# Kernel tuning notes

Measured on AMD Instinct MI355X. Metric: run time of the kernel, lower is better.

Reference implementation:

```python
import jax, jax.numpy as jnp
import numpy as np

B, S, D, H = 256, 128, 1024, 8
DH = D // H  # per-head dim = input_length / head


def setup_inputs() -> dict:
    key = jax.random.key(0)
    ks = jax.random.split(key, 12)
    code = jax.random.normal(ks[0], (B, S, D), dtype=jnp.float32)
    # 0/1 adjacency (PDG relation mask)
    input_relation = jax.random.bernoulli(ks[1], 0.2, (B, S, S)).astype(jnp.float32)
    w = 0.02
    Wq = jax.random.normal(ks[2], (H, D, DH), dtype=jnp.float32) * w
    bq = jnp.zeros((H, DH), dtype=jnp.float32)
    Wk = jax.random.normal(ks[3], (H, D, DH), dtype=jnp.float32) * w
    bk = jnp.zeros((H, DH), dtype=jnp.float32)
    Wv = jax.random.normal(ks[4], (H, D, DH), dtype=jnp.float32) * w
    bv = jnp.zeros((H, DH), dtype=jnp.float32)
    Wo = jax.random.normal(ks[5], (2 * D, D), dtype=jnp.float32) * w
    bo = jnp.zeros((D,), dtype=jnp.float32)
    return {"code": code, "input_relation": input_relation,
            "Wq": Wq, "bq": bq, "Wk": Wk, "bk": bk,
            "Wv": Wv, "bv": bv, "Wo": Wo, "bo": bo}


def reference(code, input_relation, Wq, bq, Wk, bk, Wv, bv, Wo, bo):
    Hn = Wq.shape[0]
    half = Hn // 2
    Sn = code.shape[1]
    E = jnp.eye(Sn, dtype=code.dtype)
    # Faithful to the TF loop: head i < H/2 sees relation + i*I (the loop
    # reassigns input_relation = this_relation + I each iteration);
    # heads i >= H/2 see the ORIGINAL transposed relation.
    i_idx = jnp.arange(half, dtype=code.dtype)  # [half]
    rel_fwd = input_relation[None] + i_idx[:, None, None, None] * E  # [half,B,S,S]
    rel_t = jnp.swapaxes(input_relation, 1, 2)
    rel_bwd = jnp.broadcast_to(rel_t[None], (Hn - half,) + rel_t.shape)
    rels = jnp.concatenate([rel_fwd, rel_bwd], axis=0)  # [H,B,S,S]

    relu = jax.nn.relu
    Q = relu(jnp.einsum('bsd,hdf->hbsf', code, Wq) + bq[:, None, None, :])
    K = relu(jnp.einsum('bsd,hdf->hbsf', code, Wk) + bk[:, None, None, :])
    V = relu(jnp.einsum('bsd,hdf->hbsf', code, Wv) + bv[:, None, None, :])

    attn = jnp.einsum('hbsf,hbtf->hbst', Q, K)  # [H,B,S,S]
    pdg = rels * attn + 1e-11
    # tf.reduce_sum axis=1 (rows) -> our axis=2; axis=2 (cols) -> our axis=3
    indeg = jnp.sqrt(jnp.sum(pdg, axis=2, keepdims=True))   # [H,B,1,S]
    outdeg = jnp.sqrt(jnp.sum(pdg, axis=3, keepdims=True))  # [H,B,S,1]
    pdg = pdg / indeg / outdeg
    softed = rels * pdg
    res = jnp.einsum('hbst,hbtf->hbsf', softed, V)  # [H,B,S,DH]

    # concat heads along features (head 0 first), then concat original code
    all_ch = jnp.transpose(res, (1, 2, 0, 3)).reshape(code.shape[0], Sn, -1)
    add_ori = jnp.concatenate([all_ch, code], axis=-1)  # [B,S,2D]
    out = relu(add_ori @ Wo + bo)
    return out
```

## Files before the change

### kernel.cpp

```cpp
#include <hip/hip_runtime.h>
#include <cstdint>
#include <cstddef>

#define B_  256
#define S_  128
#define D_  1024
#define H_  8
#define DH_ 128
#define M_  (B_ * S_)

typedef _Float16 half8 __attribute__((ext_vector_type(8)));
typedef float    f32x4 __attribute__((ext_vector_type(4)));

#define GLOAD_LDS16(gp, lp)                                                    \
    __builtin_amdgcn_global_load_lds(                                          \
        (const __attribute__((address_space(1))) void*)(gp),                   \
        (__attribute__((address_space(3))) void*)(lp), 16, 0, 0)

__global__ __launch_bounds__(256)
void cvt_code(const float* __restrict__ src, _Float16* __restrict__ dst, int n8)
{
    int i = blockIdx.x * 256 + threadIdx.x;
    if (i >= n8) return;
    const float4* s = (const float4*)src;
    float4 a = s[2 * i], b = s[2 * i + 1];
    half8 o;
    o[0] = (_Float16)a.x; o[1] = (_Float16)a.y; o[2] = (_Float16)a.z; o[3] = (_Float16)a.w;
    o[4] = (_Float16)b.x; o[5] = (_Float16)b.y; o[6] = (_Float16)b.z; o[7] = (_Float16)b.w;
    *(half8*)(dst + (size_t)i * 8) = o;
}

__global__ __launch_bounds__(256)
void cvt_wqkv(const float* __restrict__ Wq, const float* __restrict__ Wk,
              const float* __restrict__ Wv,
              const float* __restrict__ bq, const float* __restrict__ bk,
              const float* __restrict__ bv,
              _Float16* __restrict__ Wt, float* __restrict__ bias_all)
{
    int idx = blockIdx.x * 256 + threadIdx.x;
    if (idx >= 3072 * 128) return;
    int n = idx >> 7, kc = idx & 127, k = kc * 8;
    int qkv = n >> 10, hf = n & 1023, h = hf >> 7, f = hf & 127;
    const float* W = (qkv == 0 ? Wq : (qkv == 1 ? Wk : Wv))
                     + (size_t)h * D_ * DH_ + (size_t)k * DH_ + f;
    half8 o;
    #pragma unroll
    for (int j = 0; j < 8; ++j) o[j] = (_Float16)W[(size_t)j * DH_];
    *(half8*)(Wt + (size_t)n * 1024 + k) = o;
    if (kc == 0)
        bias_all[n] = (qkv == 0 ? bq : (qkv == 1 ? bk : bv))[h * DH_ + f];
}

__global__ __launch_bounds__(256)
void cvt_wo(const float* __restrict__ Wo, _Float16* __restrict__ Wot)
{
    int idx = blockIdx.x * 256 + threadIdx.x;
    if (idx >= 1024 * 256) return;
    int n = idx >> 8, kc = idx & 255, k = kc * 8;
    const float* W = Wo + (size_t)k * 1024 + n;
    half8 o;
    #pragma unroll
    for (int j = 0; j < 8; ++j) o[j] = (_Float16)W[(size_t)j * 1024];
    *(half8*)(Wot + (size_t)n * 2048 + k) = o;
}

template <bool OUTF32>
__global__ __launch_bounds__(256, 2)
void gemm_f16(const _Float16* __restrict__ A1, const _Float16* __restrict__ A2,
              int K1, const _Float16* __restrict__ Bt,
              const float* __restrict__ bias, void* __restrict__ outp,
              int Ntot, int Ktot)
{
    __shared__ _Float16 Ab[2][128 * 32];
    __shared__ _Float16 Bb[2][128 * 32];

    const int tid = threadIdx.x;
    const int w = tid >> 6, l = tid & 63;
    const int wr = w >> 1, wc = w & 1;
    const int m0 = blockIdx.x * 128, n0 = blockIdx.y * 128;
    const int NT = Ktot / 32;

    auto stage = [&](int buf, int t) {
        const int k0 = t * 32;
        const _Float16* Asrc; int kc;
        if (k0 < K1) { Asrc = A1; kc = k0; } else { Asrc = A2; kc = k0 - K1; }
        const int r = w * 32 + (l >> 2);
        const int c = (l & 3) * 8;
        #pragma unroll
        for (int i = 0; i < 2; ++i) {
            const _Float16* g = Asrc + (size_t)(m0 + r + i * 16) * 1024 + kc + c;
            GLOAD_LDS16(g, &Ab[buf][(w * 32 + i * 16) * 32]);
        }
        #pragma unroll
        for (int i = 0; i < 2; ++i) {
            const _Float16* g = Bt + (size_t)(n0 + r + i * 16) * Ktot + k0 + c;
            GLOAD_LDS16(g, &Bb[buf][(w * 32 + i * 16) * 32]);
        }
    };

    f32x4 acc[4][4] = {};

    stage(0, 0);
    __syncthreads();

    int buf = 0;
    for (int t = 0; t < NT; ++t) {
        if (t + 1 < NT) stage(buf ^ 1, t + 1);

        const int g = l >> 4, r = l & 15;
        half8 af[4], bf[4];
        #pragma unroll
        for (int i = 0; i < 4; ++i)
            af[i] = *(const half8*)&Ab[buf][(wr * 64 + i * 16 + r) * 32 + g * 8];
        #pragma unroll
        for (int j = 0; j < 4; ++j)
            bf[j] = *(const half8*)&Bb[buf][(wc * 64 + j * 16 + r) * 32 + g * 8];

        #pragma unroll
        for (int i = 0; i < 4; ++i)
            #pragma unroll
            for (int j = 0; j < 4; ++j)
                acc[i][j] = __builtin_amdgcn_mfma_f32_16x16x32_f16(af[i], bf[j], acc[i][j], 0, 0, 0);

        __syncthreads();
        buf ^= 1;
    }

    const int lg = l >> 4, lr = l & 15;
    #pragma unroll
    for (int i = 0; i < 4; ++i) {
        #pragma unroll
        for (int j = 0; j < 4; ++j) {
            const int n = n0 + wc * 64 + j * 16 + lr;
            const float bs = bias[n];
            #pragma unroll
            for (int rg = 0; rg < 4; ++rg) {
                const int m = m0 + wr * 64 + i * 16 + lg * 4 + rg;
                float v = acc[i][j][rg] + bs;
                v = v > 0.0f ? v : 0.0f;
                if constexpr (OUTF32)
                    ((float*)outp)[(size_t)m * Ntot + n] = v;
                else
                    ((_Float16*)outp)[(size_t)m * Ntot + n] = (_Float16)v;
            }
        }
    }
}

#define PPAD 136
#define VPAD 40

__global__ __launch_bounds__(256, 2)
void attn_pdg_mfma(const _Float16* __restrict__ QKV, const float* __restrict__ Rel,
                   _Float16* __restrict__ resh)
{
    __shared__ __align__(16) char smem[72704];
    _Float16* P     = (_Float16*)smem;
    _Float16* Qs    = (_Float16*)(smem + 34816);
    _Float16* Ks    = Qs + 2 * 4096;
    _Float16* Vt    = (_Float16*)(smem + 34816);
    unsigned* rbits = (unsigned*)(smem + 67584);
    float* rowpart  = (float*)(smem + 69632);
    float* colpart  = (float*)(smem + 70656);
    float* inv_in   = (float*)(smem + 71680);
    float* inv_out  = (float*)(smem + 72192);

    const int tid = threadIdx.x;
    const int w = tid >> 6, l = tid & 63;
    const int wr = w >> 1, wc = w & 1;
    const int lr = l & 15, lg = l >> 4;
    const int b = blockIdx.x, h = blockIdx.y;

    for (int s = w; s < S_; s += 4) {
        const float* row = &Rel[((size_t)b * S_ + s) * S_];
        unsigned long long b0 = __ballot(row[l] > 0.5f);
        unsigned long long b1 = __ballot(row[64 + l] > 0.5f);
        if (l == 0) {
            rbits[s * 4 + 0] = (unsigned)b0; rbits[s * 4 + 1] = (unsigned)(b0 >> 32);
            rbits[s * 4 + 2] = (unsigned)b1; rbits[s * 4 + 3] = (unsigned)(b1 >> 32);
        }
    }

    const size_t gbase = (size_t)(b * S_) * 3072 + h * DH_;

    auto stageQK = [&](int bufi, int t) {
        const int k0 = t * 32;
        const int rr = l >> 2, cc = (l & 3) * 8;
        #pragma unroll
        for (int i = 0; i < 2; ++i) {
            const int row = w * 32 + i * 16;
            const _Float16* gq = QKV + gbase + (size_t)(row + rr) * 3072 + k0 + cc;
            GLOAD_LDS16(gq, Qs + bufi * 4096 + row * 32);
            const _Float16* gk = QKV + gbase + 1024 + (size_t)(row + rr) * 3072 + k0 + cc;
            GLOAD_LDS16(gk, Ks + bufi * 4096 + row * 32);
        }
    };

    f32x4 acc[4][4] = {};
    stageQK(0, 0);
    __syncthreads();
    int buf = 0;
    for (int t = 0; t < 4; ++t) {
        if (t < 3) stageQK(buf ^ 1, t + 1);
        half8 af[4], bf[4];
        #pragma unroll
        for (int i = 0; i < 4; ++i)
            af[i] = *(const half8*)&Qs[buf * 4096 + (wr * 64 + i * 16 + lr) * 32 + lg * 8];
        #pragma unroll
        for (int j = 0; j < 4; ++j)
            bf[j] = *(const half8*)&Ks[buf * 4096 + (wc * 64 + j * 16 + lr) * 32 + lg * 8];
        #pragma unroll
        for (int i = 0; i < 4; ++i)
            #pragma unroll
            for (int j = 0; j < 4; ++j)
                acc[i][j] = __builtin_amdgcn_mfma_f32_16x16x32_f16(af[i], bf[j], acc[i][j], 0, 0, 0);
        __syncthreads();
        buf ^= 1;
    }

    auto relf = [&](int s, int t) -> float {
        float r;
        if (h < H_ / 2) {
            r = (float)((rbits[s * 4 + (t >> 5)] >> (t & 31)) & 1u);
            if (s == t) r += (float)h;
        } else {
            r = (float)((rbits[t * 4 + (s >> 5)] >> (s & 31)) & 1u);
        }
        return r;
    };

    f32x4 p[4][4];
    #pragma unroll
    for (int i = 0; i < 4; ++i)
        #pragma unroll
        for (int j = 0; j < 4; ++j)
            #pragma unroll
            for (int rg = 0; rg < 4; ++rg) {
                const int s = wr * 64 + i * 16 + lg * 4 + rg;
                const int t = wc * 64 + j * 16 + lr;
                p[i][j][rg] = relf(s, t) * acc[i][j][rg] + 1e-11f;
            }

    #pragma unroll
    for (int i = 0; i < 4; ++i)
        #pragma unroll
        for (int rg = 0; rg < 4; ++rg) {
            float part = p[i][0][rg] + p[i][1][rg] + p[i][2][rg] + p[i][3][rg];
            part += __shfl_xor(part, 1);
            part += __shfl_xor(part, 2);
            part += __shfl_xor(part, 4);
            part += __shfl_xor(part, 8);
            if (lr == 0) rowpart[wc * 128 + wr * 64 + i * 16 + lg * 4 + rg] = part;
        }
    #pragma unroll
    for (int j = 0; j < 4; ++j) {
        float part = 0.0f;
        #pragma unroll
        for (int i = 0; i < 4; ++i)
            part += p[i][j][0] + p[i][j][1] + p[i][j][2] + p[i][j][3];
        part += __shfl_xor(part, 16);
        part += __shfl_xor(part, 32);
        if (lg == 0) colpart[wr * 128 + wc * 64 + j * 16 + lr] = part;
    }
    __syncthreads();

    if (tid < 128) {
        inv_in[tid] = rsqrtf(colpart[tid] + colpart[128 + tid]);
    } else {
        const int s = tid - 128;
        inv_out[s] = rsqrtf(rowpart[s] + rowpart[128 + s]);
    }
    __syncthreads();

    float itj[4];
    #pragma unroll
    for (int j = 0; j < 4; ++j) itj[j] = inv_in[wc * 64 + j * 16 + lr];
    #pragma unroll
    for (int i = 0; i < 4; ++i)
        #pragma unroll
        for (int rg = 0; rg < 4; ++rg) {
            const int s = wr * 64 + i * 16 + lg * 4 + rg;
            const float os = inv_out[s];
            #pragma unroll
            for (int j = 0; j < 4; ++j) {
                const int t = wc * 64 + j * 16 + lr;
                const float val = relf(s, t) * p[i][j][rg] * itj[j] * os;
                P[s * PPAD + t] = (_Float16)val;
            }
        }

    const _Float16* Vb = QKV + gbase + 2048;
    uint4 vreg[2];
    auto loadV = [&](int t) {
        #pragma unroll
        for (int ii = 0; ii < 2; ++ii) {
            const int unit = tid + ii * 256;
            const int tt = unit & 31, fg = unit >> 5;
            vreg[ii] = *(const uint4*)&Vb[(size_t)(t * 32 + tt) * 3072 + fg * 8];
        }
    };

    loadV(0);
    f32x4 acc2[4][4] = {};
    for (int t = 0; t < 4; ++t) {
        #pragma unroll
        for (int ii = 0; ii < 2; ++ii) {
            union { uint4 u; _Float16 hh[8]; } uu;
            uu.u = vreg[ii];
            const int unit = tid + ii * 256;
            const int tt = unit & 31, fg = unit >> 5;
            #pragma unroll
            for (int e = 0; e < 8; ++e)
                Vt[(fg * 8 + e) * VPAD + tt] = uu.hh[e];
        }
        __syncthreads();
        if (t < 3) loadV(t + 1);

        half8 af[4], bf[4];
        #pragma unroll
        for (int i = 0; i < 4; ++i)
            af[i] = *(const half8*)&P[(wr * 64 + i * 16 + lr) * PPAD + t * 32 + lg * 8];
        #pragma unroll
        for (int j = 0; j < 4; ++j)
            bf[j] = *(const half8*)&Vt[(wc * 64 + j * 16 + lr) * VPAD + lg * 8];
        #pragma unroll
        for (int i = 0; i < 4; ++i)
            #pragma unroll
            for (int j = 0; j < 4; ++j)
                acc2[i][j] = __builtin_amdgcn_mfma_f32_16x16x32_f16(af[i], bf[j], acc2[i][j], 0, 0, 0);
        __syncthreads();
    }

    #pragma unroll
    for (int i = 0; i < 4; ++i)
        #pragma unroll
        for (int rg = 0; rg < 4; ++rg) {
            const int s = wr * 64 + i * 16 + lg * 4 + rg;
            #pragma unroll
            for (int j = 0; j < 4; ++j) {
                const int f = wc * 64 + j * 16 + lr;
                resh[((size_t)(b * S_ + s)) * 1024 + h * DH_ + f] = (_Float16)acc2[i][j][rg];
            }
        }
}

extern "C" void kernel_launch(void* const* d_in, const int* in_sizes, int n_in,
                              void* d_out, int out_size, void* d_ws, size_t ws_size,
                              hipStream_t stream)
{
    const float* code = (const float*)d_in[0];
    const float* Rel  = (const float*)d_in[1];
    const float* Wq   = (const float*)d_in[2];
    const float* bq   = (const float*)d_in[3];
    const float* Wk   = (const float*)d_in[4];
    const float* bk   = (const float*)d_in[5];
    const float* Wv   = (const float*)d_in[6];
    const float* bv   = (const float*)d_in[7];
    const float* Wo   = (const float*)d_in[8];
    const float* bo   = (const float*)d_in[9];
    float* out = (float*)d_out;
    (void)in_sizes; (void)n_in; (void)out_size; (void)ws_size;

    char* wsp = (char*)d_ws;
    _Float16* codeh = (_Float16*)wsp;  wsp += (size_t)M_ * 1024 * 2;
    _Float16* QKV   = (_Float16*)wsp;  wsp += (size_t)M_ * 3072 * 2;
    _Float16* resh  = (_Float16*)wsp;  wsp += (size_t)M_ * 1024 * 2;
    _Float16* Wt    = (_Float16*)wsp;  wsp += (size_t)3072 * 1024 * 2;
    _Float16* Wot   = (_Float16*)wsp;  wsp += (size_t)1024 * 2048 * 2;
    float* bias_all = (float*)wsp;     wsp += 3072 * 4;

    cvt_code<<<(M_ * 1024 / 8 + 255) / 256, 256, 0, stream>>>(code, codeh, M_ * 1024 / 8);
    cvt_wqkv<<<(3072 * 128 + 255) / 256, 256, 0, stream>>>(Wq, Wk, Wv, bq, bk, bv, Wt, bias_all);
    cvt_wo<<<(1024 * 256 + 255) / 256, 256, 0, stream>>>(Wo, Wot);

    gemm_f16<false><<<dim3(M_ / 128, 24), 256, 0, stream>>>(
        codeh, codeh, 1024, Wt, bias_all, (void*)QKV, 3072, 1024);

    attn_pdg_mfma<<<dim3(B_, H_), 256, 0, stream>>>(QKV, Rel, resh);

    gemm_f16<true><<<dim3(M_ / 128, 8), 256, 0, stream>>>(
        resh, codeh, 1024, Wot, bo, (void*)out, 1024, 2048);
}
```

Baseline: 661.9 us.

## Rewrite fp16 GEMM as 256x256 8-wave ping-pong pipeline with swizzled LDS

Replaces the 128x128 four-wave GEMM with a 256x256 tile, 512-thread kernel using BK=64 and a 128KB double-buffered LDS. The K-step is split into four quarter-phases that interleave global-to-LDS staging with MFMA blocks, using explicit vmcnt waits, barriers and s_setprio. LDS is XOR-swizzled to avoid bank conflicts, and blocks are remapped to group tiles for better L2 reuse. This aims to raise MFMA utilization and arithmetic intensity for both projection GEMMs, at the cost of one block per CU and fragile hand-tuned wait counts.

After: 568.1 us. 14.2% less time.

```diff
diff --git a/kernel.cpp b/kernel.cpp
--- a/kernel.cpp
+++ b/kernel.cpp
@@ -65,78 +65,172 @@
 }
 
 template <bool OUTF32>
-__global__ __launch_bounds__(256, 2)
-void gemm_f16(const _Float16* __restrict__ A1, const _Float16* __restrict__ A2,
-              int K1, const _Float16* __restrict__ Bt,
-              const float* __restrict__ bias, void* __restrict__ outp,
-              int Ntot, int Ktot)
-{
-    __shared__ _Float16 Ab[2][128 * 32];
-    __shared__ _Float16 Bb[2][128 * 32];
+__global__ __launch_bounds__(512, 1)
+void gemm_f16_8p(const _Float16* __restrict__ A1p, const _Float16* __restrict__ A2p,
+                 int K1, const _Float16* __restrict__ Bt,
+                 const float* __restrict__ bias, void* __restrict__ outp,
+                 int Ntot, int Ktot, int ntn)
+{
+    __shared__ __align__(16) char lds[131072];
 
     const int tid = threadIdx.x;
     const int w = tid >> 6, l = tid & 63;
-    const int wr = w >> 1, wc = w & 1;
-    const int m0 = blockIdx.x * 128, n0 = blockIdx.y * 128;
-    const int NT = Ktot / 32;
-
-    auto stage = [&](int buf, int t) {
-        const int k0 = t * 32;
-        const _Float16* Asrc; int kc;
-        if (k0 < K1) { Asrc = A1; kc = k0; } else { Asrc = A2; kc = k0 - K1; }
-        const int r = w * 32 + (l >> 2);
-        const int c = (l & 3) * 8;
-        #pragma unroll
-        for (int i = 0; i < 2; ++i) {
-            const _Float16* g = Asrc + (size_t)(m0 + r + i * 16) * 1024 + kc + c;
-            GLOAD_LDS16(g, &Ab[buf][(w * 32 + i * 16) * 32]);
-        }
-        #pragma unroll
-        for (int i = 0; i < 2; ++i) {
-            const _Float16* g = Bt + (size_t)(n0 + r + i * 16) * Ktot + k0 + c;
-            GLOAD_LDS16(g, &Bb[buf][(w * 32 + i * 16) * 32]);
-        }
-    };
-
-    f32x4 acc[4][4] = {};
-
-    stage(0, 0);
-    __syncthreads();
-
-    int buf = 0;
+    const int wm = w >> 2, wn = w & 3;
+    const int lr = l & 15, lg = l >> 4;
+
+    const int cpx = gridDim.x >> 3;
+    const int bid = blockIdx.x;
+    const int swz = (bid & 7) * cpx + (bid >> 3);
+    const int m0 = (swz / ntn) * 256, n0 = (swz % ntn) * 256;
+
+    const int NT = Ktot >> 6;
+
+    const int srow  = l >> 3;
+    const int sgcol = ((l & 7) ^ srow) * 8;
+
+    auto stageHalf = [&](int bufi, int t, int half) {
+        const int k0 = t << 6;
+        const bool isA = (half == 0) || (half == 3);
+        const int hh = (half >= 2) ? 1 : 0;
+        char* dst0 = lds + bufi * 65536 + (isA ? 0 : 32768) + hh * 16384;
+        if (isA) {
+            const _Float16* Asrc; int kc;
+            if (k0 < K1) { Asrc = A1p; kc = k0; } else { Asrc = A2p; kc = k0 - K1; }
+            #pragma unroll
+            for (int i = 0; i < 2; ++i) {
+                const int c = i * 8 + w;
+                const int row = hh * 128 + c * 8 + srow;
+                const _Float16* g = Asrc + (size_t)(m0 + row) * 1024 + kc + sgcol;
+                GLOAD_LDS16(g, dst0 + c * 1024);
+            }
+        } else {
+            #pragma unroll
+            for (int i = 0; i < 2; ++i) {
+                const int c = i * 8 + w;
+                const int row = hh * 128 + c * 8 + srow;
+                const _Float16* g = Bt + (size_t)(n0 + row) * Ktot + k0 + sgcol;
+                GLOAD_LDS16(g, dst0 + c * 1024);
+            }
+        }
+    };
+
+    auto ldA = [&](int bufi, int fi, int ks) -> half8 {
+        const int row = fi * 32 + wm * 16 + lr;
+        const int pos = (ks * 4 + lg) ^ (row & 7);
+        return *(const half8*)(lds + bufi * 65536 + row * 128 + pos * 16);
+    };
+    auto ldB = [&](int bufi, int fj, int ks) -> half8 {
+        const int row = fj * 64 + wn * 16 + lr;
+        const int pos = (ks * 4 + lg) ^ (row & 7);
+        return *(const half8*)(lds + bufi * 65536 + 32768 + row * 128 + pos * 16);
+    };
+
+    f32x4 acc[8][4] = {};
+    half8 aq[4][2], b0[2][2], b1[2][2];
+
+    stageHalf(0, 0, 0); stageHalf(0, 0, 1); stageHalf(0, 0, 2); stageHalf(0, 0, 3);
+
     for (int t = 0; t < NT; ++t) {
-        if (t + 1 < NT) stage(buf ^ 1, t + 1);
-
-        const int g = l >> 4, r = l & 15;
-        half8 af[4], bf[4];
-        #pragma unroll
-        for (int i = 0; i < 4; ++i)
-            af[i] = *(const half8*)&Ab[buf][(wr * 64 + i * 16 + r) * 32 + g * 8];
-        #pragma unroll
-        for (int j = 0; j < 4; ++j)
-            bf[j] = *(const half8*)&Bb[buf][(wc * 64 + j * 16 + r) * 32 + g * 8];
-
-        #pragma unroll
-        for (int i = 0; i < 4; ++i)
-            #pragma unroll
-            for (int j = 0; j < 4; ++j)
-                acc[i][j] = __builtin_amdgcn_mfma_f32_16x16x32_f16(af[i], bf[j], acc[i][j], 0, 0, 0);
-
-        __syncthreads();
-        buf ^= 1;
-    }
-
-    const int lg = l >> 4, lr = l & 15;
-    #pragma unroll
-    for (int i = 0; i < 4; ++i) {
-        #pragma unroll
-        for (int j = 0; j < 4; ++j) {
-            const int n = n0 + wc * 64 + j * 16 + lr;
+        const int buf = t & 1;
+        const bool nl = (t + 1 < NT);
+
+        asm volatile("s_waitcnt vmcnt(4)" ::: "memory");
+        __builtin_amdgcn_s_barrier();
+        #pragma unroll
+        for (int fi = 0; fi < 4; ++fi)
+            #pragma unroll
+            for (int ks = 0; ks < 2; ++ks)
+                aq[fi][ks] = ldA(buf, fi, ks);
+        #pragma unroll
+        for (int fj = 0; fj < 2; ++fj)
+            #pragma unroll
+            for (int ks = 0; ks < 2; ++ks)
+                b0[fj][ks] = ldB(buf, fj, ks);
+        if (nl) stageHalf(buf ^ 1, t + 1, 0);
+        asm volatile("s_waitcnt lgkmcnt(0)" ::: "memory");
+        __builtin_amdgcn_sched_barrier(0);
+        __builtin_amdgcn_s_setprio(1);
+        #pragma unroll
+        for (int ks = 0; ks < 2; ++ks)
+            #pragma unroll
+            for (int fi = 0; fi < 4; ++fi)
+                #pragma unroll
+                for (int fj = 0; fj < 2; ++fj)
+                    acc[fi][fj] = __builtin_amdgcn_mfma_f32_16x16x32_f16(
+                        aq[fi][ks], b0[fj][ks], acc[fi][fj], 0, 0, 0);
+        __builtin_amdgcn_s_setprio(0);
+        __builtin_amdgcn_s_barrier();
+
+        if (nl) asm volatile("s_waitcnt vmcnt(4)" ::: "memory");
+        else    asm volatile("s_waitcnt vmcnt(2)" ::: "memory");
+        __builtin_amdgcn_s_barrier();
+        #pragma unroll
+        for (int fj = 0; fj < 2; ++fj)
+            #pragma unroll
+            for (int ks = 0; ks < 2; ++ks)
+                b1[fj][ks] = ldB(buf, fj + 2, ks);
+        if (nl) stageHalf(buf ^ 1, t + 1, 1);
+        asm volatile("s_waitcnt lgkmcnt(0)" ::: "memory");
+        __builtin_amdgcn_sched_barrier(0);
+        __builtin_amdgcn_s_setprio(1);
+        #pragma unroll
+        for (int ks = 0; ks < 2; ++ks)
+            #pragma unroll
+            for (int fi = 0; fi < 4; ++fi)
+                #pragma unroll
+                for (int fj = 0; fj < 2; ++fj)
+                    acc[fi][fj + 2] = __builtin_amdgcn_mfma_f32_16x16x32_f16(
+                        aq[fi][ks], b1[fj][ks], acc[fi][fj + 2], 0, 0, 0);
+        __builtin_amdgcn_s_setprio(0);
+        __builtin_amdgcn_s_barrier();
+
+        if (nl) asm volatile("s_waitcnt vmcnt(4)" ::: "memory");
+        else    asm volatile("s_waitcnt vmcnt(0)" ::: "memory");
+        __builtin_amdgcn_s_barrier();
+        #pragma unroll
+        for (int fi = 0; fi < 4; ++fi)
+            #pragma unroll
+            for (int ks = 0; ks < 2; ++ks)
+                aq[fi][ks] = ldA(buf, fi + 4, ks);
+        if (nl) stageHalf(buf ^ 1, t + 1, 2);
+        asm volatile("s_waitcnt lgkmcnt(0)" ::: "memory");
+        __builtin_amdgcn_sched_barrier(0);
+        __builtin_amdgcn_s_setprio(1);
+        #pragma unroll
+        for (int ks = 0; ks < 2; ++ks)
+            #pragma unroll
+            for (int fi = 0; fi < 4; ++fi)
+                #pragma unroll
+                for (int fj = 0; fj < 2; ++fj)
+                    acc[fi + 4][fj + 2] = __builtin_amdgcn_mfma_f32_16x16x32_f16(
+                        aq[fi][ks], b1[fj][ks], acc[fi + 4][fj + 2], 0, 0, 0);
+        __builtin_amdgcn_s_setprio(0);
+        __builtin_amdgcn_s_barrier();
+
+        if (nl) stageHalf(buf ^ 1, t + 1, 3);
+        __builtin_amdgcn_s_setprio(1);
+        #pragma unroll
+        for (int ks = 0; ks < 2; ++ks)
+            #pragma unroll
+            for (int fi = 0; fi < 4; ++fi)
+                #pragma unroll
+                for (int fj = 0; fj < 2; ++fj)
+                    acc[fi + 4][fj] = __builtin_amdgcn_mfma_f32_16x16x32_f16(
+                        aq[fi][ks], b0[fj][ks], acc[fi + 4][fj], 0, 0, 0);
+        __builtin_amdgcn_s_setprio(0);
+        __builtin_amdgcn_s_barrier();
+    }
+
+    #pragma unroll
+    for (int fi = 0; fi < 8; ++fi) {
+        #pragma unroll
+        for (int fj = 0; fj < 4; ++fj) {
+            const int n = n0 + fj * 64 + wn * 16 + lr;
             const float bs = bias[n];
             #pragma unroll
             for (int rg = 0; rg < 4; ++rg) {
-                const int m = m0 + wr * 64 + i * 16 + lg * 4 + rg;
-                float v = acc[i][j][rg] + bs;
+                const int m = m0 + fi * 32 + wm * 16 + lg * 4 + rg;
+                float v = acc[fi][fj][rg] + bs;
                 v = v > 0.0f ? v : 0.0f;
                 if constexpr (OUTF32)
                     ((float*)outp)[(size_t)m * Ntot + n] = v;
@@ -373,11 +467,11 @@
     cvt_wqkv<<<(3072 * 128 + 255) / 256, 256, 0, stream>>>(Wq, Wk, Wv, bq, bk, bv, Wt, bias_all);
     cvt_wo<<<(1024 * 256 + 255) / 256, 256, 0, stream>>>(Wo, Wot);
 
-    gemm_f16<false><<<dim3(M_ / 128, 24), 256, 0, stream>>>(
-        codeh, codeh, 1024, Wt, bias_all, (void*)QKV, 3072, 1024);
+    gemm_f16_8p<false><<<(M_ / 256) * (3072 / 256), 512, 0, stream>>>(
+        codeh, codeh, 1024, Wt, bias_all, (void*)QKV, 3072, 1024, 3072 / 256);
 
     attn_pdg_mfma<<<dim3(B_, H_), 256, 0, stream>>>(QKV, Rel, resh);
 
-    gemm_f16<true><<<dim3(M_ / 128, 8), 256, 0, stream>>>(
-        resh, codeh, 1024, Wot, bo, (void*)out, 1024, 2048);
-}
+    gemm_f16_8p<true><<<(M_ / 256) * (1024 / 256), 512, 0, stream>>>(
+        resh, codeh, 1024, Wot, bo, (void*)out, 1024, 2048, 1024 / 256);
+}
```
